# Performance work log

Hardware: AMD Instinct MI355X
Metric: run time of the kernel (lower is better)

Reference implementation:

```python
import jax, jax.numpy as jnp
import numpy as np

THRESHOLD = 1.0
SLOPE = 25.0  # snntorch surrogate.fast_sigmoid default slope
BETA = 0.9

@jax.custom_vjp
def spike_fn(x):
    # Heaviside forward, fast-sigmoid surrogate backward: g / (slope*|x| + 1)^2
    return (x > 0).astype(x.dtype)

def _spike_fwd(x):
    return spike_fn(x), x

def _spike_bwd(x, g):
    return (g / (SLOPE * jnp.abs(x) + 1.0) ** 2,)

spike_fn.defvjp(_spike_fwd, _spike_bwd)


def setup_inputs() -> dict:
    key = jax.random.key(0)
    k_x, k_w1, k_b1, k_w2, k_b2 = jax.random.split(key, 5)
    B, T, F, H, O = 128, 256, 2500, 128, 2
    x = jax.random.normal(k_x, (B, T, F), dtype=jnp.float32)
    # PyTorch Linear init: U(-1/sqrt(fan_in), 1/sqrt(fan_in))
    s1 = 1.0 / np.sqrt(F)
    s2 = 1.0 / np.sqrt(H)
    W1 = jax.random.uniform(k_w1, (H, F), jnp.float32, -s1, s1)
    b1 = jax.random.uniform(k_b1, (H,), jnp.float32, -s1, s1)
    W2 = jax.random.uniform(k_w2, (O, H), jnp.float32, -s2, s2)
    b2 = jax.random.uniform(k_b2, (O,), jnp.float32, -s2, s2)
    return {"x": x, "W1": W1, "b1": b1, "W2": W2, "b2": b2}


def reference(x, W1, b1, W2, b2):
    # Module transposes to [time, batch, feat] when shape[0] < shape[1]
    if x.ndim == 3 and x.shape[0] < x.shape[1]:
        x = jnp.swapaxes(x, 0, 1)  # [T, B, F]
    T, B = x.shape[0], x.shape[1]
    H, O = W1.shape[0], W2.shape[0]

    def lif(mem, cur):
        # snntorch Leaky, reset_mechanism='subtract'; reset spike is detached
        rst = jax.lax.stop_gradient(spike_fn(mem - THRESHOLD))
        mem = BETA * mem + cur - rst * THRESHOLD
        spk = spike_fn(mem - THRESHOLD)
        return spk, mem

    def step(carry, xt):
        mem1, mem2 = carry
        cur1 = xt @ W1.T + b1            # [B, H]
        spk1, mem1 = lif(mem1, cur1)
        cur2 = spk1 @ W2.T + b2          # [B, O]
        spk2, mem2 = lif(mem2, cur2)
        return (mem1, mem2), (spk2, mem2)

    mem1_0 = jnp.zeros((B, H), x.dtype)
    mem2_0 = jnp.zeros((B, O), x.dtype)
    _, (spk_rec, mem_rec) = jax.lax.scan(step, (mem1_0, mem2_0), x)
    return spk_rec, mem_rec  # each [T, B, O]
```

## Files before the change

kernel.cpp:

```cpp
#include <hip/hip_runtime.h>

#define T_STEPS 256
#define B_SZ    128
#define F_SZ    2500
#define F4      625
#define H_SZ    128
#define O_SZ    2
#define FLAG_WINDOW 5e-5
#define CHUNK   12

__global__ __launch_bounds__(256) void k_transpose(const float* __restrict__ W1,
                                                   float* __restrict__ W1T,
                                                   int* __restrict__ nh) {
    int idx = blockIdx.x * 256 + threadIdx.x;
    if (idx < B_SZ) nh[idx] = 0;
    if (idx >= F_SZ * H_SZ) return;
    int k = idx >> 7;
    int h = idx & 127;
    W1T[idx] = W1[h * F_SZ + k];
}

__global__ __launch_bounds__(256, 2) void k_gemm(const float* __restrict__ x,
                                                 const float* __restrict__ W1T,
                                                 float* __restrict__ cur1) {
    __shared__ float Alds[32 * 64];
    __shared__ float Blds[32 * 128];

    const int t   = blockIdx.x >> 1;
    const int b0  = (blockIdx.x & 1) * 64;
    const int tid = threadIdx.x;
    const int tc  = tid & 15;
    const int tr  = tid >> 4;

    const int ac = tid & 7;
    const int ar = tid >> 3;
    const int aswz = (ac & 3) << 3;
    const int bn = tid & 31;
    const int bk = tid >> 5;

    float4 aV[2], bV[4];

    auto loadA = [&](int kb) {
        const int k = kb + ac * 4;
        const bool ok = (k < F_SZ);
        const float* p0 = x + ((size_t)(b0 + ar) * T_STEPS + t) * F_SZ + k;
        const float* p1 = x + ((size_t)(b0 + ar + 32) * T_STEPS + t) * F_SZ + k;
        aV[0] = ok ? *(const float4*)p0 : make_float4(0.f, 0.f, 0.f, 0.f);
        aV[1] = ok ? *(const float4*)p1 : make_float4(0.f, 0.f, 0.f, 0.f);
    };
    auto loadB = [&](int kb) {
        #pragma unroll
        for (int i = 0; i < 4; ++i) {
            const int k = kb + bk + 8 * i;
            bV[i] = (k < F_SZ) ? *(const float4*)(W1T + (size_t)k * H_SZ + bn * 4)
                               : make_float4(0.f, 0.f, 0.f, 0.f);
        }
    };
    auto stage = [&]() {
        const float* a0 = (const float*)&aV[0];
        const float* a1 = (const float*)&aV[1];
        #pragma unroll
        for (int c = 0; c < 4; ++c) {
            Alds[(ac * 4 + c) * 64 + (ar ^ aswz)]        = a0[c];
            Alds[(ac * 4 + c) * 64 + ((ar + 32) ^ aswz)] = a1[c];
        }
        #pragma unroll
        for (int i = 0; i < 4; ++i)
            *(float4*)(Blds + (bk + 8 * i) * 128 + bn * 4) = bV[i];
    };

    float acc0[4][4], acc1[4][4];
    #pragma unroll
    for (int i = 0; i < 4; ++i)
        #pragma unroll
        for (int j = 0; j < 4; ++j) { acc0[i][j] = 0.f; acc1[i][j] = 0.f; }

    const int NSTEP = 79;
    loadA(0);
    loadB(0);

    #pragma unroll 1
    for (int s = 0; s < NSTEP; ++s) {
        __syncthreads();
        stage();
        if (s + 1 < NSTEP) { loadA((s + 1) * 32); loadB((s + 1) * 32); }
        __syncthreads();

        #pragma unroll
        for (int k = 0; k < 32; ++k) {
            const float4 a4  = *(const float4*)(Alds + k * 64 + ((tr * 4) ^ (((k >> 2) & 3) << 3)));
            const float4 b4a = *(const float4*)(Blds + k * 128 + tc * 4);
            const float4 b4b = *(const float4*)(Blds + k * 128 + 64 + tc * 4);
            const float* af = (const float*)&a4;
            const float* ba = (const float*)&b4a;
            const float* bb = (const float*)&b4b;
            #pragma unroll
            for (int i = 0; i < 4; ++i)
                #pragma unroll
                for (int j = 0; j < 4; ++j) {
                    acc0[i][j] = fmaf(af[i], ba[j], acc0[i][j]);
                    acc1[i][j] = fmaf(af[i], bb[j], acc1[i][j]);
                }
        }
    }

    #pragma unroll
    for (int i = 0; i < 4; ++i) {
        const int bg = b0 + tr * 4 + i;
        float* op = cur1 + ((size_t)t * B_SZ + bg) * H_SZ + tc * 4;
        *(float4*)op        = make_float4(acc0[i][0], acc0[i][1], acc0[i][2], acc0[i][3]);
        *(float4*)(op + 64) = make_float4(acc1[i][0], acc1[i][1], acc1[i][2], acc1[i][3]);
    }
}

__global__ __launch_bounds__(256) void k_lif1(const float* __restrict__ cur1,
                                              const float* __restrict__ b1,
                                              unsigned long long* __restrict__ spk_bits,
                                              int* __restrict__ nh,
                                              int* __restrict__ hlist) {
    const int idx = blockIdx.x * 256 + threadIdx.x;
    const int b = idx >> 7, h = idx & 127;
    const double b1v = (double)b1[h];
    double mem = 0.0;
    bool flagged = false;
    for (int t = 0; t < T_STEPS; ++t) {
        const double cur = (double)cur1[(size_t)t * 16384 + idx] + b1v;
        const double rst = (mem > 1.0) ? 1.0 : 0.0;
        mem = fma(0.9, mem, cur) - rst;
        const bool spk = (mem > 1.0);
        const unsigned long long m = __ballot(spk);
        if ((threadIdx.x & 63) == 0)
            spk_bits[((size_t)t * B_SZ + b) * 2 + ((h >> 6) & 1)] = m;
        if (!flagged && fabs(mem - 1.0) < FLAG_WINDOW) {
            flagged = true;
            int s = atomicAdd(&nh[b], 1);
            hlist[b * 128 + s] = h;
        }
    }
}

__global__ __launch_bounds__(256) void k_cur2(const unsigned long long* __restrict__ bits,
                                              const float* __restrict__ W2,
                                              const float* __restrict__ b2,
                                              double* __restrict__ cur2) {
    __shared__ float w2s[256];
    w2s[threadIdx.x] = W2[threadIdx.x];
    __syncthreads();
    const int pair = blockIdx.x * 256 + threadIdx.x;
    unsigned long long m0 = bits[(size_t)pair * 2];
    unsigned long long m1 = bits[(size_t)pair * 2 + 1];
    double v0 = (double)b2[0], v1 = (double)b2[1];
    while (m0) {
        const int i = __ffsll((long long)m0) - 1; m0 &= m0 - 1;
        v0 += (double)w2s[i]; v1 += (double)w2s[128 + i];
    }
    while (m1) {
        const int i = __ffsll((long long)m1) - 1; m1 &= m1 - 1;
        v0 += (double)w2s[64 + i]; v1 += (double)w2s[192 + i];
    }
    cur2[(size_t)pair * 2]     = v0;
    cur2[(size_t)pair * 2 + 1] = v1;
}

__global__ __launch_bounds__(256) void k_fixA(const float* __restrict__ x,
                                              const float* __restrict__ W1,
                                              const int* __restrict__ nh,
                                              const int* __restrict__ hlist,
                                              double* __restrict__ cur_fix) {
    const int b   = blockIdx.x >> 4;
    const int tch = blockIdx.x & 15;
    const int n   = nh[b];
    if (n == 0) return;

    __shared__ float w1s[CHUNK * F_SZ];
    const int tid  = threadIdx.x;
    const int wv   = tid >> 6;
    const int lane = tid & 63;

    for (int c0 = 0; c0 < n; c0 += CHUNK) {
        const int nc = (n - c0 < CHUNK) ? (n - c0) : CHUNK;
        __syncthreads();
        for (int r = 0; r < nc; ++r) {
            const int h = hlist[b * 128 + c0 + r];
            const float4* src = (const float4*)W1 + (size_t)h * F4;
            float4* dst = (float4*)(w1s + r * F_SZ);
            for (int c = tid; c < F4; c += 256) dst[c] = src[c];
        }
        __syncthreads();

        #pragma unroll 1
        for (int tt = 0; tt < 4; ++tt) {
            const int t = tch * 16 + wv * 4 + tt;
            float4 xv[10];
            const float4* xb = (const float4*)x + ((size_t)b * T_STEPS + t) * F4;
            #pragma unroll
            for (int j = 0; j < 10; ++j) {
                const int c = lane + 64 * j;
                xv[j] = (c < F4) ? xb[c] : make_float4(0.f, 0.f, 0.f, 0.f);
            }
            for (int s = 0; s < nc; ++s) {
                const float* wr = w1s + s * F_SZ;
                double p = 0.0;
                #pragma unroll
                for (int j = 0; j < 10; ++j) {
                    const int c = lane + 64 * j;
                    if (c < F4) {
                        const float4 w4 = *(const float4*)(wr + c * 4);
                        p = fma((double)xv[j].x, (double)w4.x, p);
                        p = fma((double)xv[j].y, (double)w4.y, p);
                        p = fma((double)xv[j].z, (double)w4.z, p);
                        p = fma((double)xv[j].w, (double)w4.w, p);
                    }
                }
                #pragma unroll
                for (int off = 32; off >= 1; off >>= 1) p += __shfl_down(p, off);
                if (lane == 0)
                    cur_fix[((size_t)b * 128 + c0 + s) * T_STEPS + t] = p;
            }
        }
    }
}

__global__ __launch_bounds__(128) void k_fixB(const float* __restrict__ cur1,
                                              const double* __restrict__ cur_fix,
                                              const float* __restrict__ b1,
                                              const float* __restrict__ W2,
                                              const int* __restrict__ nh,
                                              const int* __restrict__ hlist,
                                              double* __restrict__ cur2) {
    const int b = blockIdx.x;
    const int s = threadIdx.x;
    if (s >= nh[b]) return;
    const int h = hlist[b * 128 + s];
    const double b1v = (double)b1[h];
    const double w0 = (double)W2[h], w1 = (double)W2[128 + h];
    double ma = 0.0, me = 0.0;
    for (int t = 0; t < T_STEPS; ++t) {
        const double ca = (double)cur1[((size_t)t * B_SZ + b) * H_SZ + h] + b1v;
        const double ce = cur_fix[((size_t)b * 128 + s) * T_STEPS + t] + b1v;
        const double ra = (ma > 1.0) ? 1.0 : 0.0;
        const double re = (me > 1.0) ? 1.0 : 0.0;
        ma = fma(0.9, ma, ca) - ra;
        me = fma(0.9, me, ce) - re;
        const bool sa = (ma > 1.0), se = (me > 1.0);
        if (sa != se) {
            const double d = se ? 1.0 : -1.0;
            atomicAdd(&cur2[((size_t)t * B_SZ + b) * 2 + 0], d * w0);
            atomicAdd(&cur2[((size_t)t * B_SZ + b) * 2 + 1], d * w1);
        }
    }
}

__global__ __launch_bounds__(256) void k_lif2(const double* __restrict__ cur2,
                                              float* __restrict__ out) {
    const int tid = threadIdx.x;
    double mem = 0.0;
    float* spk_out = out;
    float* mem_out = out + T_STEPS * B_SZ * O_SZ;
    #pragma unroll 8
    for (int t = 0; t < T_STEPS; ++t) {
        const double cur = cur2[t * 256 + tid];
        const double rst = (mem > 1.0) ? 1.0 : 0.0;
        mem = fma(0.9, mem, cur) - rst;
        spk_out[t * 256 + tid] = (mem > 1.0) ? 1.0f : 0.0f;
        mem_out[t * 256 + tid] = (float)mem;
    }
}

extern "C" void kernel_launch(void* const* d_in, const int* in_sizes, int n_in,
                              void* d_out, int out_size, void* d_ws, size_t ws_size,
                              hipStream_t stream) {
    const float* x  = (const float*)d_in[0];
    const float* W1 = (const float*)d_in[1];
    const float* b1 = (const float*)d_in[2];
    const float* W2 = (const float*)d_in[3];
    const float* b2 = (const float*)d_in[4];
    float* out = (float*)d_out;

    char* ws = (char*)d_ws;
    float*  cur1     = (float*)ws;
    float*  W1T      = (float*)(ws + 16777216);
    double* cur2     = (double*)(ws + 18057216);
    double* cur_fix  = (double*)(ws + 18581504);
    int*    nh       = (int*)(ws + 52135936);
    int*    hlist    = (int*)(ws + 52136448);
    unsigned long long* spk_bits = (unsigned long long*)(ws + 52201984);

    k_transpose<<<1250, 256, 0, stream>>>(W1, W1T, nh);
    k_gemm<<<512, 256, 0, stream>>>(x, W1T, cur1);
    k_lif1<<<64, 256, 0, stream>>>(cur1, b1, spk_bits, nh, hlist);
    k_cur2<<<128, 256, 0, stream>>>(spk_bits, W2, b2, cur2);
    k_fixA<<<2048, 256, 0, stream>>>(x, W1, nh, hlist, cur_fix);
    k_fixB<<<128, 128, 0, stream>>>(cur1, cur_fix, b1, W2, nh, hlist, cur2);
    k_lif2<<<1, 256, 0, stream>>>(cur2, out);
}
```

Before: 836.5 us.

## Move layer-1 GEMM to bf16 MFMA with hi/lo split and double-buffered LDS

Replaces the FP32 FMA tiled GEMM for x·W1ᵀ with bf16 MFMA instructions (16x16x32). It emulates FP32 accuracy by splitting both x and W1 into high and low bf16 parts and running four MFMAs per tile pair. W1 is pre-split once into padded hi/lo bf16 arrays in place of the old transpose. LDS is double-buffered so global loads of the next tile overlap the current MFMAs. The fixup flag window is widened to absorb the extra rounding error, which can send more neurons through the fixup path; workspace offsets are rearranged and spk_bits now shares memory with cur_fix.

```diff
diff --git a/kernel.cpp b/kernel.cpp
--- a/kernel.cpp
+++ b/kernel.cpp
@@ -4,113 +4,176 @@
 #define B_SZ    128
 #define F_SZ    2500
 #define F4      625
+#define F_P     2528
+#define NSTEP   79
 #define H_SZ    128
 #define O_SZ    2
-#define FLAG_WINDOW 5e-5
+#define FLAG_WINDOW 8e-5
 #define CHUNK   12
 
-__global__ __launch_bounds__(256) void k_transpose(const float* __restrict__ W1,
-                                                   float* __restrict__ W1T,
-                                                   int* __restrict__ nh) {
-    int idx = blockIdx.x * 256 + threadIdx.x;
-    if (idx < B_SZ) nh[idx] = 0;
-    if (idx >= F_SZ * H_SZ) return;
-    int k = idx >> 7;
-    int h = idx & 127;
-    W1T[idx] = W1[h * F_SZ + k];
+typedef unsigned short U16;
+typedef short  s16x8 __attribute__((ext_vector_type(8)));
+typedef U16    u16x8 __attribute__((ext_vector_type(8)));
+typedef float  f32x4 __attribute__((ext_vector_type(4)));
+
+__device__ __forceinline__ U16 bf16_rne(float f) {
+    unsigned u = __float_as_uint(f);
+    u += 0x7FFFu + ((u >> 16) & 1u);
+    return (U16)(u >> 16);
+}
+
+__global__ __launch_bounds__(256) void k_split(const float* __restrict__ W1,
+                                               U16* __restrict__ W1h,
+                                               U16* __restrict__ W1l,
+                                               int* __restrict__ nh) {
+    const int h = blockIdx.x;
+    if (h == 0 && threadIdx.x < B_SZ) nh[threadIdx.x] = 0;
+    for (int k = threadIdx.x; k < F_P; k += 256) {
+        const float w = (k < F_SZ) ? W1[(size_t)h * F_SZ + k] : 0.f;
+        const U16 hi = bf16_rne(w);
+        const float hf = __uint_as_float((unsigned)hi << 16);
+        W1h[(size_t)h * F_P + k] = hi;
+        W1l[(size_t)h * F_P + k] = bf16_rne(w - hf);
+    }
 }
 
 __global__ __launch_bounds__(256, 2) void k_gemm(const float* __restrict__ x,
-                                                 const float* __restrict__ W1T,
+                                                 const U16* __restrict__ W1h,
+                                                 const U16* __restrict__ W1l,
                                                  float* __restrict__ cur1) {
-    __shared__ float Alds[32 * 64];
-    __shared__ float Blds[32 * 128];
-
+    __shared__ __align__(16) U16 Alds[2][128 * 64];
+    __shared__ __align__(16) U16 Blds[2][64 * 64];
+
+    const int tid = threadIdx.x;
     const int t   = blockIdx.x >> 1;
-    const int b0  = (blockIdx.x & 1) * 64;
-    const int tid = threadIdx.x;
-    const int tc  = tid & 15;
-    const int tr  = tid >> 4;
-
-    const int ac = tid & 7;
-    const int ar = tid >> 3;
-    const int aswz = (ac & 3) << 3;
-    const int bn = tid & 31;
-    const int bk = tid >> 5;
-
-    float4 aV[2], bV[4];
-
-    auto loadA = [&](int kb) {
-        const int k = kb + ac * 4;
-        const bool ok = (k < F_SZ);
-        const float* p0 = x + ((size_t)(b0 + ar) * T_STEPS + t) * F_SZ + k;
-        const float* p1 = x + ((size_t)(b0 + ar + 32) * T_STEPS + t) * F_SZ + k;
-        aV[0] = ok ? *(const float4*)p0 : make_float4(0.f, 0.f, 0.f, 0.f);
-        aV[1] = ok ? *(const float4*)p1 : make_float4(0.f, 0.f, 0.f, 0.f);
-    };
-    auto loadB = [&](int kb) {
-        #pragma unroll
-        for (int i = 0; i < 4; ++i) {
-            const int k = kb + bk + 8 * i;
-            bV[i] = (k < F_SZ) ? *(const float4*)(W1T + (size_t)k * H_SZ + bn * 4)
-                               : make_float4(0.f, 0.f, 0.f, 0.f);
-        }
-    };
-    auto stage = [&]() {
-        const float* a0 = (const float*)&aV[0];
-        const float* a1 = (const float*)&aV[1];
-        #pragma unroll
-        for (int c = 0; c < 4; ++c) {
-            Alds[(ac * 4 + c) * 64 + (ar ^ aswz)]        = a0[c];
-            Alds[(ac * 4 + c) * 64 + ((ar + 32) ^ aswz)] = a1[c];
-        }
-        #pragma unroll
-        for (int i = 0; i < 4; ++i)
-            *(float4*)(Blds + (bk + 8 * i) * 128 + bn * 4) = bV[i];
-    };
-
-    float acc0[4][4], acc1[4][4];
+    const int h0  = (blockIdx.x & 1) << 6;
+
+    const int ra   = tid >> 1;
+    const int kq   = (tid & 1) << 4;
+    const int aswz = ra & 7;
+    const int au0  = (tid & 1) << 1;
+    const float* xp = x + ((size_t)ra * T_STEPS + t) * F_SZ + kq;
+
+    const int rb  = tid >> 2;
+    const int ub0 = (tid & 3) << 1;
+    const U16* bsrc[2];
+    #pragma unroll
+    for (int c = 0; c < 2; ++c) {
+        const int lu = (ub0 + c) ^ (rb & 7);
+        const U16* base = (lu < 4) ? (W1h + lu * 8) : (W1l + (lu - 4) * 8);
+        bsrc[c] = base + (size_t)(h0 + rb) * F_P;
+    }
+
+    const int wid = tid >> 6, lane = tid & 63;
+    const int wm0 = (wid >> 1) << 6;
+    const int wn0 = (wid & 1) << 5;
+    const int lr = lane & 15, lg = lane >> 4;
+
+    f32x4 acc[4][2];
     #pragma unroll
     for (int i = 0; i < 4; ++i)
         #pragma unroll
-        for (int j = 0; j < 4; ++j) { acc0[i][j] = 0.f; acc1[i][j] = 0.f; }
-
-    const int NSTEP = 79;
-    loadA(0);
+        for (int j = 0; j < 2; ++j) {
+            acc[i][j][0] = 0.f; acc[i][j][1] = 0.f; acc[i][j][2] = 0.f; acc[i][j][3] = 0.f;
+        }
+
+    float4 xr[4];
+    u16x8  br[2];
+
+    auto loadX = [&](int kk) {
+        #pragma unroll
+        for (int c = 0; c < 4; ++c) {
+            const int k = kk + kq + c * 4;
+            xr[c] = (k < F_SZ) ? *(const float4*)(xp + kk + c * 4)
+                               : make_float4(0.f, 0.f, 0.f, 0.f);
+        }
+    };
+    auto loadB = [&](int kk) {
+        #pragma unroll
+        for (int c = 0; c < 2; ++c) br[c] = *(const u16x8*)(bsrc[c] + kk);
+    };
+    auto stage = [&](int bb) {
+        U16* Ab = Alds[bb];
+        U16* Bb = Blds[bb];
+        u16x8 vh[2], vl[2];
+        #pragma unroll
+        for (int p = 0; p < 2; ++p) {
+            const float* f0 = (const float*)&xr[p * 2];
+            const float* f1 = (const float*)&xr[p * 2 + 1];
+            #pragma unroll
+            for (int j = 0; j < 4; ++j) {
+                const float v0 = f0[j], v1 = f1[j];
+                const U16 hv0 = bf16_rne(v0);
+                const U16 hv1 = bf16_rne(v1);
+                vh[p][j]     = hv0;
+                vh[p][4 + j] = hv1;
+                vl[p][j]     = bf16_rne(v0 - __uint_as_float((unsigned)hv0 << 16));
+                vl[p][4 + j] = bf16_rne(v1 - __uint_as_float((unsigned)hv1 << 16));
+            }
+        }
+        #pragma unroll
+        for (int p = 0; p < 2; ++p) {
+            *(u16x8*)(Ab + ra * 64 + (((au0 + p) ^ aswz) << 3))       = vh[p];
+            *(u16x8*)(Ab + ra * 64 + (((au0 + p + 4) ^ aswz) << 3))   = vl[p];
+        }
+        #pragma unroll
+        for (int c = 0; c < 2; ++c)
+            *(u16x8*)(Bb + rb * 64 + ((ub0 + c) << 3)) = br[c];
+    };
+
+    loadX(0);
     loadB(0);
-
+    stage(0);
+
+    int bb = 0;
     #pragma unroll 1
     for (int s = 0; s < NSTEP; ++s) {
         __syncthreads();
-        stage();
-        if (s + 1 < NSTEP) { loadA((s + 1) * 32); loadB((s + 1) * 32); }
-        __syncthreads();
-
-        #pragma unroll
-        for (int k = 0; k < 32; ++k) {
-            const float4 a4  = *(const float4*)(Alds + k * 64 + ((tr * 4) ^ (((k >> 2) & 3) << 3)));
-            const float4 b4a = *(const float4*)(Blds + k * 128 + tc * 4);
-            const float4 b4b = *(const float4*)(Blds + k * 128 + 64 + tc * 4);
-            const float* af = (const float*)&a4;
-            const float* ba = (const float*)&b4a;
-            const float* bb = (const float*)&b4b;
+        const bool more = (s + 1 < NSTEP);
+        if (more) { loadX((s + 1) * 32); loadB((s + 1) * 32); }
+
+        const U16* Ab = Alds[bb];
+        const U16* Bb = Blds[bb];
+        s16x8 ah[4], al[4], bh[2], blo[2];
+        #pragma unroll
+        for (int fi = 0; fi < 4; ++fi) {
+            const int m = wm0 + fi * 16 + lr;
+            const int msw = m & 7;
+            ah[fi] = *(const s16x8*)(Ab + m * 64 + ((lg ^ msw) << 3));
+            al[fi] = *(const s16x8*)(Ab + m * 64 + (((lg + 4) ^ msw) << 3));
+        }
+        #pragma unroll
+        for (int fj = 0; fj < 2; ++fj) {
+            const int n = wn0 + fj * 16 + lr;
+            const int nsw = n & 7;
+            bh[fj]  = *(const s16x8*)(Bb + n * 64 + ((lg ^ nsw) << 3));
+            blo[fj] = *(const s16x8*)(Bb + n * 64 + (((lg + 4) ^ nsw) << 3));
+        }
+        #pragma unroll
+        for (int fi = 0; fi < 4; ++fi)
             #pragma unroll
-            for (int i = 0; i < 4; ++i)
-                #pragma unroll
-                for (int j = 0; j < 4; ++j) {
-                    acc0[i][j] = fmaf(af[i], ba[j], acc0[i][j]);
-                    acc1[i][j] = fmaf(af[i], bb[j], acc1[i][j]);
-                }
-        }
+            for (int fj = 0; fj < 2; ++fj) {
+                acc[fi][fj] = __builtin_amdgcn_mfma_f32_16x16x32_bf16(ah[fi], bh[fj],  acc[fi][fj], 0, 0, 0);
+                acc[fi][fj] = __builtin_amdgcn_mfma_f32_16x16x32_bf16(ah[fi], blo[fj], acc[fi][fj], 0, 0, 0);
+                acc[fi][fj] = __builtin_amdgcn_mfma_f32_16x16x32_bf16(al[fi], bh[fj],  acc[fi][fj], 0, 0, 0);
+                acc[fi][fj] = __builtin_amdgcn_mfma_f32_16x16x32_bf16(al[fi], blo[fj], acc[fi][fj], 0, 0, 0);
+            }
+
+        if (more) stage(bb ^ 1);
+        bb ^= 1;
     }
 
     #pragma unroll
-    for (int i = 0; i < 4; ++i) {
-        const int bg = b0 + tr * 4 + i;
-        float* op = cur1 + ((size_t)t * B_SZ + bg) * H_SZ + tc * 4;
-        *(float4*)op        = make_float4(acc0[i][0], acc0[i][1], acc0[i][2], acc0[i][3]);
-        *(float4*)(op + 64) = make_float4(acc1[i][0], acc1[i][1], acc1[i][2], acc1[i][3]);
-    }
+    for (int fi = 0; fi < 4; ++fi)
+        #pragma unroll
+        for (int fj = 0; fj < 2; ++fj) {
+            const int hcol = h0 + wn0 + fj * 16 + lr;
+            #pragma unroll
+            for (int r = 0; r < 4; ++r) {
+                const int brow = wm0 + fi * 16 + lg * 4 + r;
+                cur1[((size_t)t * B_SZ + brow) * H_SZ + hcol] = acc[fi][fj][r];
+            }
+        }
 }
 
 __global__ __launch_bounds__(256) void k_lif1(const float* __restrict__ cur1,
@@ -123,6 +186,7 @@
     const double b1v = (double)b1[h];
     double mem = 0.0;
     bool flagged = false;
+    #pragma unroll 4
     for (int t = 0; t < T_STEPS; ++t) {
         const double cur = (double)cur1[(size_t)t * 16384 + idx] + b1v;
         const double rst = (mem > 1.0) ? 1.0 : 0.0;
@@ -278,16 +342,17 @@
     float* out = (float*)d_out;
 
     char* ws = (char*)d_ws;
-    float*  cur1     = (float*)ws;
-    float*  W1T      = (float*)(ws + 16777216);
-    double* cur2     = (double*)(ws + 18057216);
-    double* cur_fix  = (double*)(ws + 18581504);
-    int*    nh       = (int*)(ws + 52135936);
-    int*    hlist    = (int*)(ws + 52136448);
-    unsigned long long* spk_bits = (unsigned long long*)(ws + 52201984);
-
-    k_transpose<<<1250, 256, 0, stream>>>(W1, W1T, nh);
-    k_gemm<<<512, 256, 0, stream>>>(x, W1T, cur1);
+    float*  cur1    = (float*)ws;
+    U16*    W1h     = (U16*)(ws + 16777216);
+    U16*    W1l     = (U16*)(ws + 17424384);
+    double* cur2    = (double*)(ws + 18071552);
+    double* cur_fix = (double*)(ws + 18595840);
+    unsigned long long* spk_bits = (unsigned long long*)(ws + 18595840);
+    int*    nh      = (int*)(ws + 52150272);
+    int*    hlist   = (int*)(ws + 52150784);
+
+    k_split<<<128, 256, 0, stream>>>(W1, W1h, W1l, nh);
+    k_gemm<<<512, 256, 0, stream>>>(x, W1h, W1l, cur1);
     k_lif1<<<64, 256, 0, stream>>>(cur1, b1, spk_bits, nh, hlist);
     k_cur2<<<128, 256, 0, stream>>>(spk_bits, W2, b2, cur2);
     k_fixA<<<2048, 256, 0, stream>>>(x, W1, nh, hlist, cur_fix);
```

After: 789.5 us. 5.6% less time.
